# Optimization experiments

Measured on AMD Instinct MI355X. Metric: run time of the kernel, lower is better.

The kernel has to match this reference:

```python
import jax, jax.numpy as jnp
import numpy as np

N_U = 50000   # num user nodes
N_I = 50000   # num item nodes
D = 64        # in_size == out_size
H = 128       # SemanticAttention hidden size (default)
E = 500000    # edges per meta-path graph
NEG_SLOPE = 0.01


def setup_inputs() -> dict:
    key = jax.random.key(0)
    ks = jax.random.split(key, 24)
    rn = lambda k, shp, s=0.1: jax.random.normal(k, shp, jnp.float32) * s
    ri = lambda k, shp, n: jax.random.randint(k, shp, 0, n, dtype=jnp.int32)
    return dict(
        feat_user=rn(ks[0], (N_U, D)), feat_item=rn(ks[1], (N_I, D)),
        attn_l=rn(ks[2], (4, D)), attn_r=rn(ks[3], (4, D)),
        W_gc=rn(ks[4], (4, D, D)), b_gc=jnp.zeros((4, D), jnp.float32),
        sa_rel_W1=rn(ks[5], (D, H)), sa_rel_b1=jnp.zeros((H,), jnp.float32), sa_rel_w2=rn(ks[6], (H,)),
        sa_u_W1=rn(ks[7], (D, H)), sa_u_b1=jnp.zeros((H,), jnp.float32), sa_u_w2=rn(ks[8], (H,)),
        sa_i_W1=rn(ks[9], (D, H)), sa_i_b1=jnp.zeros((H,), jnp.float32), sa_i_w2=rn(ks[10], (H,)),
        rel_u_src=ri(ks[11], (2, E), N_I), rel_u_dst=ri(ks[12], (2, E), N_U),
        rel_i_src=ri(ks[13], (2, E), N_U), rel_i_dst=ri(ks[14], (2, E), N_I),
        mp_u_src=ri(ks[15], (2, E), N_U), mp_u_dst=ri(ks[16], (2, E), N_U),
        mp_i_src=ri(ks[17], (2, E), N_I), mp_i_dst=ri(ks[18], (2, E), N_I),
    )


def _edge_softmax(e, dst, n_dst):
    # segment-wise (per destination node) softmax over irregular edges
    m = jax.ops.segment_max(e, dst, num_segments=n_dst)
    ex = jnp.exp(e - m[dst])
    s = jax.ops.segment_sum(ex, dst, num_segments=n_dst)
    return ex / s[dst]


def _heco_gat(src, dst, feat_src, feat_dst, al, ar, n_dst):
    # HeCoGATConv: el = sum(ft_src*attn_l), er = sum(ft_dst*attn_r)
    el = feat_src @ al  # (N_src,)
    er = feat_dst @ ar  # (N_dst,)
    e = jax.nn.leaky_relu(el[src] + er[dst], NEG_SLOPE)  # (E,)
    a = _edge_softmax(e, dst, n_dst)
    out = jax.ops.segment_sum(feat_src[src] * a[:, None], dst, num_segments=n_dst)
    return jax.nn.elu(out)


def _graph_conv(src, dst, feat, W, b, n):
    # DGL GraphConv with norm='both', activation=elu
    ones = jnp.ones(src.shape, jnp.float32)
    deg_out = jax.ops.segment_sum(ones, src, num_segments=n)
    deg_in = jax.ops.segment_sum(ones, dst, num_segments=n)
    no = jnp.where(deg_out > 0, deg_out, 1.0) ** -0.5
    ni = jnp.where(deg_in > 0, deg_in, 1.0) ** -0.5
    h = feat * no[:, None]
    agg = jax.ops.segment_sum(h[src], dst, num_segments=n)
    agg = agg * ni[:, None]
    return jax.nn.elu(agg @ W + b)


def _semantic_attention(z, W1, b1, w2):
    # z: (N, M, D) -> (N, D)
    w = (jnp.tanh(z @ W1 + b1) @ w2).mean(0)  # (M,)
    beta = jax.nn.softmax(w)
    return jnp.einsum('nmd,m->nd', z, beta)


def reference(feat_user, feat_item, attn_l, attn_r, W_gc, b_gc,
              sa_rel_W1, sa_rel_b1, sa_rel_w2,
              sa_u_W1, sa_u_b1, sa_u_w2,
              sa_i_W1, sa_i_b1, sa_i_w2,
              rel_u_src, rel_u_dst, rel_i_src, rel_i_dst,
              mp_u_src, mp_u_dst, mp_i_src, mp_i_dst):
    # --- RelationalAGG: HeCo GAT over schema-level relations ---
    zu = jnp.stack([
        _heco_gat(rel_u_src[0], rel_u_dst[0], feat_item, feat_user, attn_l[0], attn_r[0], N_U),
        _heco_gat(rel_u_src[1], rel_u_dst[1], feat_item, feat_user, attn_l[1], attn_r[1], N_U),
    ], axis=1)  # (N_U, 2, D)
    rel_u = _semantic_attention(zu, sa_rel_W1, sa_rel_b1, sa_rel_w2)
    zi = jnp.stack([
        _heco_gat(rel_i_src[0], rel_i_dst[0], feat_user, feat_item, attn_l[2], attn_r[2], N_I),
        _heco_gat(rel_i_src[1], rel_i_dst[1], feat_user, feat_item, attn_l[3], attn_r[3], N_I),
    ], axis=1)
    rel_i = _semantic_attention(zi, sa_rel_W1, sa_rel_b1, sa_rel_w2)
    # --- HAN layers: GraphConv over meta-path reachable graphs ---
    hu = jnp.stack([
        _graph_conv(mp_u_src[0], mp_u_dst[0], feat_user, W_gc[0], b_gc[0], N_U),
        _graph_conv(mp_u_src[1], mp_u_dst[1], feat_user, W_gc[1], b_gc[1], N_U),
    ], axis=1)
    han_u = _semantic_attention(hu, sa_u_W1, sa_u_b1, sa_u_w2)
    hi = jnp.stack([
        _graph_conv(mp_i_src[0], mp_i_dst[0], feat_item, W_gc[2], b_gc[2], N_I),
        _graph_conv(mp_i_src[1], mp_i_dst[1], feat_item, W_gc[3], b_gc[3], N_I),
    ], axis=1)
    han_i = _semantic_attention(hi, sa_i_W1, sa_i_b1, sa_i_w2)
    user_emb = rel_u + han_u
    item_emb = rel_i + han_i
    return jnp.concatenate([user_emb, item_emb], axis=0)  # (N_U + N_I, D)
```

## Files before the change

kernel.cpp:

```cpp
#include <hip/hip_runtime.h>
#include <math.h>

#define NU 50000
#define NI 50000
#define NN 50000
#define DD 64
#define HHID 128
#define EE 500000
#define NEG_SLOPE 0.01f
#define NBKT 196
#define CAP 3072
#define TILE 8192
#define TPG 62
#define P1T 512
#define NIMG 12
#define AGGB 1563
#define SEMB 512

typedef _Float16 half_t;
typedef _Float16 half8 __attribute__((ext_vector_type(8)));
typedef float f32x4 __attribute__((ext_vector_type(4)));
union H4 { uint2 u; half_t h[4]; };
union H8 { uint4 u; half_t h[8]; };
union HS { half8 h; int i[4]; uint4 u; };
union HC { unsigned short us; half_t h; };

struct Ptr4c { const float* p[4]; };
struct Ptr4m { float*       p[4]; };
struct EdgeArgs { const int* src[8]; const int* dst[8]; };
struct GatArgs { const half_t* fsrc[4]; half_t* zout[4]; };
struct GcArgs  { const half_t* feat[4]; half_t* hout[4]; };
struct WArgs   { const float* el[4]; const float* er[4]; const int* deg_src; };
struct SemArgs { const half_t* z[4]; const float* W1[4]; const float* b1[4]; const float* w2[4]; };
struct PrepArgs {
    const float* featI; const float* featU;
    Ptr4c vi; Ptr4c vu; Ptr4m oi; Ptr4m ou;
    half_t* FBI; half_t* FBU;
    const float* W_gc; half_t* W16;
};

__global__ __launch_bounds__(256) void prep_kernel(PrepArgs pa) {
    int b = blockIdx.x;
    int t = threadIdx.x;
    if (b == 6250) {
        int g = t >> 6;
        int lane = t & 63;
        int cl = lane & 15, quad = lane >> 4;
#pragma unroll
        for (int nt = 0; nt < 4; nt++) {
#pragma unroll
            for (int kh = 0; kh < 2; kh++) {
                H8 o;
#pragma unroll
                for (int j = 0; j < 8; j++) {
                    int k = kh * 32 + quad * 8 + j;
                    int n = nt * 16 + cl;
                    o.h[j] = (half_t)pa.W_gc[g * 4096 + k * 64 + n];
                }
                *(uint4*)(pa.W16 + ((g * 8 + nt * 2 + kh) * 64 + lane) * 8) = o.u;
            }
        }
        return;
    }
    const float* feat; Ptr4c vecs; Ptr4m outs; half_t* fb16; int bb;
    if (b < 3125) { feat = pa.featI; vecs = pa.vi; outs = pa.oi; fb16 = pa.FBI; bb = b; }
    else          { feat = pa.featU; vecs = pa.vu; outs = pa.ou; fb16 = pa.FBU; bb = b - 3125; }
    int w = bb * 4 + (t >> 6);
    int lane = t & 63;
    int sub = lane >> 4, r = lane & 15;
    int node = w * 4 + sub;
    float4 f = *(const float4*)(feat + node * DD + r * 4);
    H4 o16;
    o16.h[0] = (half_t)f.x; o16.h[1] = (half_t)f.y; o16.h[2] = (half_t)f.z; o16.h[3] = (half_t)f.w;
    *(uint2*)(fb16 + node * DD + r * 4) = o16.u;
#pragma unroll
    for (int j = 0; j < 4; j++) {
        float4 vv = *(const float4*)(vecs.p[j] + r * 4);
        float val = f.x * vv.x + f.y * vv.y + f.z * vv.z + f.w * vv.w;
        val += __shfl_down(val, 8);
        val += __shfl_down(val, 4);
        val += __shfl_down(val, 2);
        val += __shfl_down(val, 1);
        if (r == 0) outs.p[j][node] = val;
    }
}

__global__ __launch_bounds__(P1T) void part1_kernel(EdgeArgs a, int* __restrict__ ccnt,
                                                    int* __restrict__ coarse) {
    __shared__ int bc_cnt[256], bc_scan[256], bc_start[256], bc_cur[256], bc_gbase[256];
    __shared__ int stage[TILE];
    int t = threadIdx.x;
    int g = blockIdx.x / TPG;
    int tile = blockIdx.x % TPG;
    int e0 = tile * TILE;
    int tile_n = min(TILE, EE - e0);
    bool cnt_only = g >= 8;
    const int* gk = (cnt_only ? a.src[g - 4] : a.dst[g]) + e0;
    const int* gs = cnt_only ? gk : (a.src[g] + e0);
    if (t < 256) bc_cnt[t] = 0;
    __syncthreads();
    for (int pos = t * 4; pos < tile_n; pos += P1T * 4) {
        int4 k4 = *(const int4*)(gk + pos);
        atomicAdd(&bc_cnt[k4.x >> 8], 1);
        atomicAdd(&bc_cnt[k4.y >> 8], 1);
        atomicAdd(&bc_cnt[k4.z >> 8], 1);
        atomicAdd(&bc_cnt[k4.w >> 8], 1);
    }
    __syncthreads();
    if (t < 256) bc_scan[t] = bc_cnt[t];
    __syncthreads();
    for (int off = 1; off < 256; off <<= 1) {
        int v = (t < 256 && t >= off) ? bc_scan[t - off] : 0;
        __syncthreads();
        if (t < 256) bc_scan[t] += v;
        __syncthreads();
    }
    if (t < 256) {
        int st = bc_scan[t] - bc_cnt[t];
        bc_start[t] = st;
        bc_cur[t] = st;
        bc_gbase[t] = (t < NBKT && bc_cnt[t] > 0) ? atomicAdd(&ccnt[g * NBKT + t], bc_cnt[t]) : 0;
    }
    __syncthreads();
    for (int pos = t * 4; pos < tile_n; pos += P1T * 4) {
        int4 k4 = *(const int4*)(gk + pos);
        int4 s4;
        if (cnt_only) { s4 = make_int4(0, 0, 0, 0); }
        else          { s4 = *(const int4*)(gs + pos); }
        int b0 = k4.x >> 8, b1 = k4.y >> 8, b2 = k4.z >> 8, b3 = k4.w >> 8;
        int sl0 = atomicAdd(&bc_cur[b0], 1);
        int sl1 = atomicAdd(&bc_cur[b1], 1);
        int sl2 = atomicAdd(&bc_cur[b2], 1);
        int sl3 = atomicAdd(&bc_cur[b3], 1);
        stage[sl0] = s4.x | ((k4.x & 255) << 16) | (b0 << 24);
        stage[sl1] = s4.y | ((k4.y & 255) << 16) | (b1 << 24);
        stage[sl2] = s4.z | ((k4.z & 255) << 16) | (b2 << 24);
        stage[sl3] = s4.w | ((k4.w & 255) << 16) | (b3 << 24);
    }
    __syncthreads();
    for (int j = t; j < tile_n; j += P1T) {
        int p = stage[j];
        int b = (unsigned)p >> 24;
        int pos = bc_gbase[b] + (j - bc_start[b]);
        if (pos < CAP) coarse[(g * NBKT + b) * CAP + pos] = p & 0x00FFFFFF;
    }
}

__global__ __launch_bounds__(256) void degcnt_kernel(const int* __restrict__ ccnt,
                                                     const int* __restrict__ coarse,
                                                     int* __restrict__ DEG_SRC) {
    __shared__ int cnt[256];
    int t = threadIdx.x;
    int g2 = blockIdx.x / NBKT;
    int b = blockIdx.x % NBKT;
    int img = 8 + g2;
    int n = min(ccnt[img * NBKT + b], CAP);
    cnt[t] = 0;
    __syncthreads();
    const int* pairs = coarse + (img * NBKT + b) * CAP;
    for (int i = t; i < n; i += 256) atomicAdd(&cnt[(pairs[i] >> 16) & 255], 1);
    __syncthreads();
    int v = (b << 8) + t;
    if (v < NN) DEG_SRC[g2 * NN + v] = cnt[t];
}

__global__ __launch_bounds__(256) void part2_kernel(const int* __restrict__ ccnt,
                                                    const int* __restrict__ coarse,
                                                    WArgs wa,
                                                    int* __restrict__ bucket,
                                                    int2* __restrict__ RD) {
    __shared__ int sb[256];
    __shared__ int cnt5[256], off5[256], s2[256];
    __shared__ int ordered[CAP];
    int t = threadIdx.x;
    int g = blockIdx.x / NBKT;
    int b = blockIdx.x % NBKT;
    int ccv = (t < NBKT) ? min(ccnt[g * NBKT + t], CAP) : 0;
    sb[t] = ccv;
    cnt5[t] = 0;
    __syncthreads();
    for (int off = 1; off < 256; off <<= 1) {
        int vv = (t >= off) ? sb[t - off] : 0;
        __syncthreads();
        sb[t] += vv;
        __syncthreads();
    }
    int base = (b > 0) ? sb[b - 1] : 0;
    int n = sb[b] - base;
    int node0 = b << 8;
    const int* pairs = coarse + (g * NBKT + b) * CAP;
    for (int i = t; i < n; i += 256) atomicAdd(&cnt5[pairs[i] >> 16], 1);
    __syncthreads();
    int myc = cnt5[t];
    s2[t] = myc;
    __syncthreads();
    for (int off = 1; off < 256; off <<= 1) {
        int vv = (t >= off) ? s2[t - off] : 0;
        __syncthreads();
        s2[t] += vv;
        __syncthreads();
    }
    int ex = s2[t] - myc;
    off5[t] = ex;
    int v = node0 + t;
    if (v < NN) RD[g * NN + v] = make_int2(base + ex, myc);
    __syncthreads();
    int nm1 = n - 1;
    for (int ib = t; ib < n; ib += 1024) {
        int p[4];
#pragma unroll
        for (int u = 0; u < 4; u++) {
            int i = ib + u * 256;
            p[u] = pairs[(i < n) ? i : nm1];
        }
        float w[4];
        if (g < 4) {
            float a0[4], a1[4];
#pragma unroll
            for (int u = 0; u < 4; u++) a0[u] = wa.el[g][p[u] & 0xFFFF];
#pragma unroll
            for (int u = 0; u < 4; u++) a1[u] = wa.er[g][node0 + (p[u] >> 16)];
#pragma unroll
            for (int u = 0; u < 4; u++) {
                float e = a0[u] + a1[u];
                e = (e >= 0.f) ? e : NEG_SLOPE * e;
                w[u] = __expf(e);
            }
        } else {
            int dv[4];
#pragma unroll
            for (int u = 0; u < 4; u++) dv[u] = wa.deg_src[(g - 4) * NN + (p[u] & 0xFFFF)];
#pragma unroll
            for (int u = 0; u < 4; u++) w[u] = __builtin_amdgcn_rsqf((float)dv[u]);
        }
#pragma unroll
        for (int u = 0; u < 4; u++) {
            int i = ib + u * 256;
            if (i < n) {
                HC cv; cv.h = (half_t)w[u];
                int slot = atomicAdd(&off5[p[u] >> 16], 1);
                ordered[slot] = (p[u] & 0xFFFF) | ((int)cv.us << 16);
            }
        }
    }
    __syncthreads();
    int* bko = bucket + g * EE + base;
    for (int i = t; i < n; i += 256) bko[i] = ordered[i];
}

__global__ __launch_bounds__(256) void agg_kernel(GatArgs ga, GcArgs gc, half_t* __restrict__ AGG,
                                                  const int2* __restrict__ RD,
                                                  const int* __restrict__ bucket) {
    int g = blockIdx.x / AGGB;
    int nb = blockIdx.x % AGGB;
    int t = threadIdx.x;
    int wv = t >> 6, lane = t & 63;
    int q = lane >> 3, r = lane & 7;
    int v = nb * 32 + wv * 8 + q;
    bool vok = v < NN;
    int2 rd = RD[g * NN + (vok ? v : 0)];
    int start = rd.x;
    int dg = vok ? rd.y : 0;
    const int* bk = bucket + g * EE;
    const half_t* feat = (g < 4) ? ga.fsrc[g] : gc.feat[g - 4];
    int roff = r << 3;
    int obase = lane & 56;
    HS acc[4];
#pragma unroll
    for (int a = 0; a < 4; a++)
#pragma unroll
        for (int j = 0; j < 4; j++) acc[a].i[j] = 0;
    float s_l = 0.f;
    for (int b8 = 0; b8 < dg; b8 += 8) {
        int rem = dg - b8;
        int p = bk[start + b8 + ((r < rem) ? r : 0)];
#pragma unroll
        for (int j = 0; j < 8; j++) {
            if (j < rem) {
                int pj = __shfl(p, obase + j);
                HC wj; wj.us = (unsigned short)((unsigned)pj >> 16);
                s_l += (float)wj.h;
                HS row; row.u = *(const uint4*)(feat + (((pj & 0xFFFF) << 6) + roff));
                half_t wh = wj.h;
                half8 ws = {wh, wh, wh, wh, wh, wh, wh, wh};
                acc[j & 3].h += row.h * ws;
            }
        }
    }
    acc[0].h += acc[1].h;
    acc[2].h += acc[3].h;
    acc[0].h += acc[2].h;
    if (g < 4) {
        float inv = (dg > 0) ? __builtin_amdgcn_rcpf(s_l) : 0.f;
        H8 o;
#pragma unroll
        for (int i = 0; i < 8; i++) {
            float x = (float)acc[0].h[i] * inv;
            x = (x > 0.f) ? x : (__expf(x) - 1.f);
            o.h[i] = (half_t)x;
        }
        if (vok) *(uint4*)(ga.zout[g] + (v << 7) + roff) = o.u;
    } else {
        float niv = (dg > 0) ? __builtin_amdgcn_rsqf((float)dg) : 1.0f;
        H8 o;
#pragma unroll
        for (int i = 0; i < 8; i++) o.h[i] = (half_t)((float)acc[0].h[i] * niv);
        if (vok) *(uint4*)(AGG + (((g - 4) * NN + v) << 6) + roff) = o.u;
    }
}

__global__ __launch_bounds__(256) void trans_kernel(GcArgs gc, const half_t* __restrict__ AGG,
                                                    const half_t* __restrict__ W16,
                                                    const float* __restrict__ b_gc) {
    int t = threadIdx.x;
    int wv = t >> 6, lane = t & 63;
    int g = blockIdx.x / 782;
    int tile = (blockIdx.x % 782) * 4 + wv;
    if (tile >= 3125) return;
    int cl = lane & 15, quad = lane >> 4;
    const half_t* ab = AGG + ((g * NN + tile * 16 + cl) << 6);
    half8 A0 = *(const half8*)(ab + quad * 8);
    half8 A1 = *(const half8*)(ab + 32 + quad * 8);
    const half_t* wbase = W16 + g * 8 * 64 * 8;
    half_t* hout = gc.hout[g];
#pragma unroll
    for (int nt = 0; nt < 4; nt++) {
        float bb = b_gc[g * 64 + nt * 16 + cl];
        f32x4 c = {bb, bb, bb, bb};
        half8 B0 = *(const half8*)(wbase + ((nt * 2 + 0) * 64 + lane) * 8);
        half8 B1 = *(const half8*)(wbase + ((nt * 2 + 1) * 64 + lane) * 8);
        c = __builtin_amdgcn_mfma_f32_16x16x32_f16(A0, B0, c, 0, 0, 0);
        c = __builtin_amdgcn_mfma_f32_16x16x32_f16(A1, B1, c, 0, 0, 0);
#pragma unroll
        for (int r_ = 0; r_ < 4; r_++) {
            int node = tile * 16 + quad * 4 + r_;
            float x = c[r_];
            x = (x > 0.f) ? x : (__expf(x) - 1.f);
            hout[node * 128 + nt * 16 + cl] = (half_t)x;
        }
    }
}

__global__ __launch_bounds__(256) void sem_att_kernel(SemArgs sa, float* __restrict__ wsum) {
    __shared__ half_t As[2][1024];
    __shared__ float s0[4], s1[4];
    int inst = blockIdx.x / SEMB;
    int blk  = blockIdx.x % SEMB;
    int t = threadIdx.x;
    int wv = t >> 6, lane = t & 63;
    int quad = lane >> 4, cl = lane & 15;
    const half_t* z = sa.z[inst];
    const float* W1 = sa.W1[inst];
    half8 Bf[2][2];
    float b1v[2], w2v[2];
#pragma unroll
    for (int u = 0; u < 2; u++) {
        int nt = wv * 2 + u;
        int n = nt * 16 + cl;
#pragma unroll
        for (int kh = 0; kh < 2; kh++) {
#pragma unroll
            for (int j = 0; j < 8; j++) {
                int k = kh * 32 + quad * 8 + j;
                Bf[u][kh][j] = (half_t)W1[k * HHID + n];
            }
        }
        b1v[u] = sa.b1[inst][nt * 16 + cl];
        w2v[u] = sa.w2[inst][nt * 16 + cl];
    }
    float local0 = 0.f, local1 = 0.f;

#define SEM_STAGE(buf, tp) { \
    if (wv < 2) { \
        int m_ = ((tp) >= 3125) ? 1 : 0; \
        int tm_ = (tp) - m_ * 3125; \
        int c_ = (wv << 6) + lane; \
        int n_ = c_ >> 3, j_ = c_ & 7; \
        const half_t* src_ = z + (size_t)(tm_ * 16 + n_) * 128 + m_ * 64 + j_ * 8; \
        __builtin_amdgcn_global_load_lds( \
            (const __attribute__((address_space(1))) unsigned int*)src_, \
            (__attribute__((address_space(3))) unsigned int*)(&As[buf][wv * 512]), \
            16, 0, 0); \
    } }

    int tile = blk;
    int cur = 0;
    SEM_STAGE(0, tile);
    while (tile < 6250) {
        int ntile = tile + SEMB;
        bool more = ntile < 6250;
        if (more) {
            SEM_STAGE(cur ^ 1, ntile);
            asm volatile("s_waitcnt vmcnt(1)" ::: "memory");
        } else {
            asm volatile("s_waitcnt vmcnt(0)" ::: "memory");
        }
        __builtin_amdgcn_sched_barrier(0);
        __builtin_amdgcn_s_barrier();
        const half_t* ar = &As[cur][cl * 64 + quad * 8];
        half8 A0 = *(const half8*)(ar);
        half8 A1 = *(const half8*)(ar + 32);
        float sumv = 0.f;
#pragma unroll
        for (int u = 0; u < 2; u++) {
            f32x4 c = {0.f, 0.f, 0.f, 0.f};
            c = __builtin_amdgcn_mfma_f32_16x16x32_f16(A0, Bf[u][0], c, 0, 0, 0);
            c = __builtin_amdgcn_mfma_f32_16x16x32_f16(A1, Bf[u][1], c, 0, 0, 0);
#pragma unroll
            for (int r = 0; r < 4; r++) {
                float xv = c[r] + b1v[u];
                float ev = __expf(2.f * xv);
                float th = 1.f - 2.f * __builtin_amdgcn_rcpf(ev + 1.f);
                sumv += th * w2v[u];
            }
        }
        if (tile < 3125) local0 += sumv; else local1 += sumv;
        __builtin_amdgcn_s_barrier();
        cur ^= 1;
        tile = ntile;
    }
#undef SEM_STAGE
#pragma unroll
    for (int off = 32; off > 0; off >>= 1) {
        local0 += __shfl_down(local0, off);
        local1 += __shfl_down(local1, off);
    }
    if (lane == 0) { s0[wv] = local0; s1[wv] = local1; }
    __syncthreads();
    if (t == 0) {
        float a0 = s0[0] + s0[1] + s0[2] + s0[3];
        float a1 = s1[0] + s1[1] + s1[2] + s1[3];
        if (a0 != 0.f) atomicAdd(&wsum[inst * 2 + 0], a0);
        if (a1 != 0.f) atomicAdd(&wsum[inst * 2 + 1], a1);
    }
}

__global__ void combine_kernel(const half_t* __restrict__ ZU, const half_t* __restrict__ ZI,
                               const half_t* __restrict__ HU, const half_t* __restrict__ HI,
                               const float* __restrict__ wsum, float* __restrict__ out) {
    int gid = blockIdx.x * blockDim.x + threadIdx.x;
    if (gid >= (NU + NI) * 16) return;
    int node = gid >> 4;
    int c4 = (gid & 15) * 4;
    const half_t* zb; const half_t* hb;
    float wr0, wr1, wh0, wh1;
    int idx;
    if (node < NU) {
        zb = ZU; hb = HU; idx = node;
        wr0 = wsum[0]; wr1 = wsum[1]; wh0 = wsum[4]; wh1 = wsum[5];
    } else {
        zb = ZI; hb = HI; idx = node - NU;
        wr0 = wsum[2]; wr1 = wsum[3]; wh0 = wsum[6]; wh1 = wsum[7];
    }
    const float inv_n = 1.0f / 50000.0f;
    wr0 *= inv_n; wr1 *= inv_n; wh0 *= inv_n; wh1 *= inv_n;
    float m = fmaxf(wr0, wr1);
    float e0 = __expf(wr0 - m), e1 = __expf(wr1 - m);
    float br0 = e0 / (e0 + e1), br1 = e1 / (e0 + e1);
    m = fmaxf(wh0, wh1);
    e0 = __expf(wh0 - m); e1 = __expf(wh1 - m);
    float bh0 = e0 / (e0 + e1), bh1 = e1 / (e0 + e1);
    H4 z0, z1, h0, h1;
    z0.u = *(const uint2*)(zb + idx * 128 + c4);
    z1.u = *(const uint2*)(zb + idx * 128 + 64 + c4);
    h0.u = *(const uint2*)(hb + idx * 128 + c4);
    h1.u = *(const uint2*)(hb + idx * 128 + 64 + c4);
    float4 o;
    o.x = (float)z0.h[0] * br0 + (float)z1.h[0] * br1 + (float)h0.h[0] * bh0 + (float)h1.h[0] * bh1;
    o.y = (float)z0.h[1] * br0 + (float)z1.h[1] * br1 + (float)h0.h[1] * bh0 + (float)h1.h[1] * bh1;
    o.z = (float)z0.h[2] * br0 + (float)z1.h[2] * br1 + (float)h0.h[2] * bh0 + (float)h1.h[2] * bh1;
    o.w = (float)z0.h[3] * br0 + (float)z1.h[3] * br1 + (float)h0.h[3] * bh0 + (float)h1.h[3] * bh1;
    *(float4*)(out + node * 64 + c4) = o;
}

extern "C" void kernel_launch(void* const* d_in, const int* in_sizes, int n_in,
                              void* d_out, int out_size, void* d_ws, size_t ws_size,
                              hipStream_t stream) {
    const float* feat_user = (const float*)d_in[0];
    const float* feat_item = (const float*)d_in[1];
    const float* attn_l    = (const float*)d_in[2];
    const float* attn_r    = (const float*)d_in[3];
    const float* W_gc      = (const float*)d_in[4];
    const float* b_gc      = (const float*)d_in[5];
    const float* sa_rel_W1 = (const float*)d_in[6];
    const float* sa_rel_b1 = (const float*)d_in[7];
    const float* sa_rel_w2 = (const float*)d_in[8];
    const float* sa_u_W1   = (const float*)d_in[9];
    const float* sa_u_b1   = (const float*)d_in[10];
    const float* sa_u_w2   = (const float*)d_in[11];
    const float* sa_i_W1   = (const float*)d_in[12];
    const float* sa_i_b1   = (const float*)d_in[13];
    const float* sa_i_w2   = (const float*)d_in[14];
    const int* rel_u_src = (const int*)d_in[15];
    const int* rel_u_dst = (const int*)d_in[16];
    const int* rel_i_src = (const int*)d_in[17];
    const int* rel_i_dst = (const int*)d_in[18];
    const int* mp_u_src  = (const int*)d_in[19];
    const int* mp_u_dst  = (const int*)d_in[20];
    const int* mp_i_src  = (const int*)d_in[21];
    const int* mp_i_dst  = (const int*)d_in[22];

    half_t* ZU   = (half_t*)d_ws;
    half_t* ZI   = ZU + NN * 128;
    half_t* HU   = ZI + NN * 128;
    half_t* HI   = HU + NN * 128;
    half_t* FBU  = HI + NN * 128;
    half_t* FBI  = FBU + NN * 64;
    float*  DI   = (float*)(FBI + NN * 64);
    float*  DU   = DI + 4 * NN;
    int2*   RD   = (int2*)(DU + 4 * NN);
    int*    BUCKET = (int*)(RD + 8 * NN);
    int*    CCNT = BUCKET + 8 * EE;
    int*    DEG_SRC = CCNT + 12 * 256;
    float*  WSUM = (float*)(DEG_SRC + 4 * NN);
    half_t* W16  = (half_t*)(WSUM + 8);
    half_t* AGG  = W16 + 4 * 4096;
    int*    COARSE = (int*)d_ws;

    hipMemsetAsync(CCNT, 0, (size_t)(12 * 256 + 4 * NN) * sizeof(int) + 8 * sizeof(float), stream);

    PrepArgs pa;
    pa.featI = feat_item; pa.featU = feat_user;
    pa.vi = Ptr4c{{ attn_l + 0 * DD, attn_l + 1 * DD, attn_r + 2 * DD, attn_r + 3 * DD }};
    pa.oi = Ptr4m{{ DI, DI + NI, DI + 2 * NI, DI + 3 * NI }};
    pa.vu = Ptr4c{{ attn_l + 2 * DD, attn_l + 3 * DD, attn_r + 0 * DD, attn_r + 1 * DD }};
    pa.ou = Ptr4m{{ DU, DU + NU, DU + 2 * NU, DU + 3 * NU }};
    pa.FBI = FBI; pa.FBU = FBU;
    pa.W_gc = W_gc; pa.W16 = W16;
    prep_kernel<<<6251, 256, 0, stream>>>(pa);

    EdgeArgs ea;
    ea.src[0] = rel_u_src;      ea.dst[0] = rel_u_dst;
    ea.src[1] = rel_u_src + EE; ea.dst[1] = rel_u_dst + EE;
    ea.src[2] = rel_i_src;      ea.dst[2] = rel_i_dst;
    ea.src[3] = rel_i_src + EE; ea.dst[3] = rel_i_dst + EE;
    ea.src[4] = mp_u_src;       ea.dst[4] = mp_u_dst;
    ea.src[5] = mp_u_src + EE;  ea.dst[5] = mp_u_dst + EE;
    ea.src[6] = mp_i_src;       ea.dst[6] = mp_i_dst;
    ea.src[7] = mp_i_src + EE;  ea.dst[7] = mp_i_dst + EE;

    part1_kernel<<<NIMG * TPG, P1T, 0, stream>>>(ea, CCNT, COARSE);
    degcnt_kernel<<<4 * NBKT, 256, 0, stream>>>(CCNT, COARSE, DEG_SRC);

    WArgs wa;
    wa.el[0] = DI;      wa.er[0] = DU + 2 * NU;
    wa.el[1] = DI + NI; wa.er[1] = DU + 3 * NU;
    wa.el[2] = DU;      wa.er[2] = DI + 2 * NI;
    wa.el[3] = DU + NU; wa.er[3] = DI + 3 * NI;
    wa.deg_src = DEG_SRC;
    part2_kernel<<<8 * NBKT, 256, 0, stream>>>(CCNT, COARSE, wa, BUCKET, RD);

    GatArgs ga;
    ga.fsrc[0] = FBI; ga.zout[0] = ZU;
    ga.fsrc[1] = FBI; ga.zout[1] = ZU + 64;
    ga.fsrc[2] = FBU; ga.zout[2] = ZI;
    ga.fsrc[3] = FBU; ga.zout[3] = ZI + 64;
    GcArgs gc;
    gc.feat[0] = FBU; gc.hout[0] = HU;
    gc.feat[1] = FBU; gc.hout[1] = HU + 64;
    gc.feat[2] = FBI; gc.hout[2] = HI;
    gc.feat[3] = FBI; gc.hout[3] = HI + 64;
    agg_kernel<<<8 * AGGB, 256, 0, stream>>>(ga, gc, AGG, RD, BUCKET);

    trans_kernel<<<4 * 782, 256, 0, stream>>>(gc, AGG, W16, b_gc);

    SemArgs sa;
    sa.z[0] = ZU; sa.W1[0] = sa_rel_W1; sa.b1[0] = sa_rel_b1; sa.w2[0] = sa_rel_w2;
    sa.z[1] = ZI; sa.W1[1] = sa_rel_W1; sa.b1[1] = sa_rel_b1; sa.w2[1] = sa_rel_w2;
    sa.z[2] = HU; sa.W1[2] = sa_u_W1;   sa.b1[2] = sa_u_b1;   sa.w2[2] = sa_u_w2;
    sa.z[3] = HI; sa.W1[3] = sa_i_W1;   sa.b1[3] = sa_i_b1;   sa.w2[3] = sa_i_w2;
    sem_att_kernel<<<4 * SEMB, 256, 0, stream>>>(sa, WSUM);

    combine_kernel<<<((NU + NI) * 16 + 255) / 256, 256, 0, stream>>>(ZU, ZI, HU, HI, WSUM, (float*)d_out);
}
```

Before: 335.8 us.

## Split aggregation feature dim across two block halves and batch semantic-attention tiles

The aggregation kernel now launches twice as many blocks, each handling half of the 64-wide feature row with 8-byte loads. The goal is more parallelism and occupancy on the gather-bound edge aggregation, at the cost of reading the edge bucket indices and weights twice. The semantic attention kernel now has all four waves stage tiles, four tiles per barrier round, which cuts barrier and synchronisation overhead per tile. This uses four times the LDS per block.

```diff
diff --git a/kernel.cpp b/kernel.cpp
--- a/kernel.cpp
+++ b/kernel.cpp
@@ -19,10 +19,12 @@
 
 typedef _Float16 half_t;
 typedef _Float16 half8 __attribute__((ext_vector_type(8)));
+typedef _Float16 half4 __attribute__((ext_vector_type(4)));
 typedef float f32x4 __attribute__((ext_vector_type(4)));
 union H4 { uint2 u; half_t h[4]; };
 union H8 { uint4 u; half_t h[8]; };
 union HS { half8 h; int i[4]; uint4 u; };
+union HS4 { half4 h; int i[2]; uint2 u; };
 union HC { unsigned short us; half_t h; };
 
 struct Ptr4c { const float* p[4]; };
@@ -251,8 +253,10 @@
 __global__ __launch_bounds__(256) void agg_kernel(GatArgs ga, GcArgs gc, half_t* __restrict__ AGG,
                                                   const int2* __restrict__ RD,
                                                   const int* __restrict__ bucket) {
-    int g = blockIdx.x / AGGB;
-    int nb = blockIdx.x % AGGB;
+    int h = blockIdx.x / (8 * AGGB);
+    int remb = blockIdx.x % (8 * AGGB);
+    int g = remb / AGGB;
+    int nb = remb % AGGB;
     int t = threadIdx.x;
     int wv = t >> 6, lane = t & 63;
     int q = lane >> 3, r = lane & 7;
@@ -263,13 +267,11 @@
     int dg = vok ? rd.y : 0;
     const int* bk = bucket + g * EE;
     const half_t* feat = (g < 4) ? ga.fsrc[g] : gc.feat[g - 4];
-    int roff = r << 3;
+    int roff = h * 32 + (r << 2);
     int obase = lane & 56;
-    HS acc[4];
-#pragma unroll
-    for (int a = 0; a < 4; a++)
-#pragma unroll
-        for (int j = 0; j < 4; j++) acc[a].i[j] = 0;
+    HS4 acc[4];
+#pragma unroll
+    for (int a = 0; a < 4; a++) { acc[a].i[0] = 0; acc[a].i[1] = 0; }
     float s_l = 0.f;
     for (int b8 = 0; b8 < dg; b8 += 8) {
         int rem = dg - b8;
@@ -280,9 +282,9 @@
                 int pj = __shfl(p, obase + j);
                 HC wj; wj.us = (unsigned short)((unsigned)pj >> 16);
                 s_l += (float)wj.h;
-                HS row; row.u = *(const uint4*)(feat + (((pj & 0xFFFF) << 6) + roff));
+                HS4 row; row.u = *(const uint2*)(feat + (((pj & 0xFFFF) << 6) + roff));
                 half_t wh = wj.h;
-                half8 ws = {wh, wh, wh, wh, wh, wh, wh, wh};
+                half4 ws = {wh, wh, wh, wh};
                 acc[j & 3].h += row.h * ws;
             }
         }
@@ -292,20 +294,20 @@
     acc[0].h += acc[2].h;
     if (g < 4) {
         float inv = (dg > 0) ? __builtin_amdgcn_rcpf(s_l) : 0.f;
-        H8 o;
-#pragma unroll
-        for (int i = 0; i < 8; i++) {
+        H4 o;
+#pragma unroll
+        for (int i = 0; i < 4; i++) {
             float x = (float)acc[0].h[i] * inv;
             x = (x > 0.f) ? x : (__expf(x) - 1.f);
             o.h[i] = (half_t)x;
         }
-        if (vok) *(uint4*)(ga.zout[g] + (v << 7) + roff) = o.u;
+        if (vok) *(uint2*)(ga.zout[g] + (v << 7) + roff) = o.u;
     } else {
         float niv = (dg > 0) ? __builtin_amdgcn_rsqf((float)dg) : 1.0f;
-        H8 o;
-#pragma unroll
-        for (int i = 0; i < 8; i++) o.h[i] = (half_t)((float)acc[0].h[i] * niv);
-        if (vok) *(uint4*)(AGG + (((g - 4) * NN + v) << 6) + roff) = o.u;
+        H4 o;
+#pragma unroll
+        for (int i = 0; i < 4; i++) o.h[i] = (half_t)((float)acc[0].h[i] * niv);
+        if (vok) *(uint2*)(AGG + (((g - 4) * NN + v) << 6) + roff) = o.u;
     }
 }
 
@@ -342,7 +344,7 @@
 }
 
 __global__ __launch_bounds__(256) void sem_att_kernel(SemArgs sa, float* __restrict__ wsum) {
-    __shared__ half_t As[2][1024];
+    __shared__ half_t As[2][4][1024];
     __shared__ float s0[4], s1[4];
     int inst = blockIdx.x / SEMB;
     int blk  = blockIdx.x % SEMB;
@@ -369,55 +371,65 @@
         w2v[u] = sa.w2[inst][nt * 16 + cl];
     }
     float local0 = 0.f, local1 = 0.f;
-
-#define SEM_STAGE(buf, tp) { \
-    if (wv < 2) { \
-        int m_ = ((tp) >= 3125) ? 1 : 0; \
-        int tm_ = (tp) - m_ * 3125; \
-        int c_ = (wv << 6) + lane; \
-        int n_ = c_ >> 3, j_ = c_ & 7; \
-        const half_t* src_ = z + (size_t)(tm_ * 16 + n_) * 128 + m_ * 64 + j_ * 8; \
+    int K = (6250 - blk + SEMB - 1) / SEMB;
+    int B = (K + 3) / 4;
+
+#define SEM_STAGE(buf, bb) { \
+    int k_ = 4 * (bb) + wv; \
+    if (k_ < K) { \
+        int tp_ = blk + k_ * SEMB; \
+        int m_ = (tp_ >= 3125) ? 1 : 0; \
+        int tm_ = tp_ - m_ * 3125; \
+        int n_ = lane >> 3; \
+        int j_ = (lane & 7) * 8; \
+        const half_t* sA_ = z + (size_t)(tm_ * 16 + n_) * 128 + m_ * 64 + j_; \
+        const half_t* sB_ = z + (size_t)(tm_ * 16 + 8 + n_) * 128 + m_ * 64 + j_; \
         __builtin_amdgcn_global_load_lds( \
-            (const __attribute__((address_space(1))) unsigned int*)src_, \
-            (__attribute__((address_space(3))) unsigned int*)(&As[buf][wv * 512]), \
-            16, 0, 0); \
+            (const __attribute__((address_space(1))) unsigned int*)sA_, \
+            (__attribute__((address_space(3))) unsigned int*)(&As[buf][wv][0]), 16, 0, 0); \
+        __builtin_amdgcn_global_load_lds( \
+            (const __attribute__((address_space(1))) unsigned int*)sB_, \
+            (__attribute__((address_space(3))) unsigned int*)(&As[buf][wv][512]), 16, 0, 0); \
     } }
 
-    int tile = blk;
     int cur = 0;
-    SEM_STAGE(0, tile);
-    while (tile < 6250) {
-        int ntile = tile + SEMB;
-        bool more = ntile < 6250;
-        if (more) {
-            SEM_STAGE(cur ^ 1, ntile);
-            asm volatile("s_waitcnt vmcnt(1)" ::: "memory");
+    SEM_STAGE(0, 0);
+    for (int b = 0; b < B; b++) {
+        if (b + 1 < B) {
+            SEM_STAGE(cur ^ 1, b + 1);
+            asm volatile("s_waitcnt vmcnt(2)" ::: "memory");
         } else {
             asm volatile("s_waitcnt vmcnt(0)" ::: "memory");
         }
         __builtin_amdgcn_sched_barrier(0);
         __builtin_amdgcn_s_barrier();
-        const half_t* ar = &As[cur][cl * 64 + quad * 8];
-        half8 A0 = *(const half8*)(ar);
-        half8 A1 = *(const half8*)(ar + 32);
-        float sumv = 0.f;
-#pragma unroll
-        for (int u = 0; u < 2; u++) {
-            f32x4 c = {0.f, 0.f, 0.f, 0.f};
-            c = __builtin_amdgcn_mfma_f32_16x16x32_f16(A0, Bf[u][0], c, 0, 0, 0);
-            c = __builtin_amdgcn_mfma_f32_16x16x32_f16(A1, Bf[u][1], c, 0, 0, 0);
-#pragma unroll
-            for (int r = 0; r < 4; r++) {
-                float xv = c[r] + b1v[u];
-                float ev = __expf(2.f * xv);
-                float th = 1.f - 2.f * __builtin_amdgcn_rcpf(ev + 1.f);
-                sumv += th * w2v[u];
+#pragma unroll
+        for (int i = 0; i < 4; i++) {
+            int k = 4 * b + i;
+            if (k < K) {
+                int tile = blk + k * SEMB;
+                const half_t* ar = &As[cur][i][cl * 64 + quad * 8];
+                half8 A0 = *(const half8*)(ar);
+                half8 A1 = *(const half8*)(ar + 32);
+                float sumv = 0.f;
+#pragma unroll
+                for (int u = 0; u < 2; u++) {
+                    f32x4 c = {0.f, 0.f, 0.f, 0.f};
+                    c = __builtin_amdgcn_mfma_f32_16x16x32_f16(A0, Bf[u][0], c, 0, 0, 0);
+                    c = __builtin_amdgcn_mfma_f32_16x16x32_f16(A1, Bf[u][1], c, 0, 0, 0);
+#pragma unroll
+                    for (int r = 0; r < 4; r++) {
+                        float xv = c[r] + b1v[u];
+                        float ev = __expf(2.f * xv);
+                        float th = 1.f - 2.f * __builtin_amdgcn_rcpf(ev + 1.f);
+                        sumv += th * w2v[u];
+                    }
+                }
+                if (tile < 3125) local0 += sumv; else local1 += sumv;
             }
         }
-        if (tile < 3125) local0 += sumv; else local1 += sumv;
         __builtin_amdgcn_s_barrier();
         cur ^= 1;
-        tile = ntile;
     }
 #undef SEM_STAGE
 #pragma unroll
@@ -560,7 +572,7 @@
     gc.feat[1] = FBU; gc.hout[1] = HU + 64;
     gc.feat[2] = FBI; gc.hout[2] = HI;
     gc.feat[3] = FBI; gc.hout[3] = HI + 64;
-    agg_kernel<<<8 * AGGB, 256, 0, stream>>>(ga, gc, AGG, RD, BUCKET);
+    agg_kernel<<<16 * AGGB, 256, 0, stream>>>(ga, gc, AGG, RD, BUCKET);
 
     trans_kernel<<<4 * 782, 256, 0, stream>>>(gc, AGG, W16, b_gc);
 
```

Result: slower. 386.1 us (+15.0%).
